# Kernel tuning notes

Hardware: AMD Instinct MI355X
Metric: run time of the kernel (lower is better)

Reference implementation:

```python
import jax, jax.numpy as jnp
import numpy as np

BETA = 0.9       # membrane decay factor
THRESHOLD = 1.0  # firing threshold
ALPHA = 2.0      # atan surrogate slope (snntorch default)

@jax.custom_vjp
def spike(x):
    # Heaviside spike on (mem - threshold)
    return (x > 0).astype(x.dtype)

def _spike_fwd(x):
    return (x > 0).astype(x.dtype), x

def _spike_bwd(x, g):
    # atan surrogate: d spk / d x = (alpha/2) / (1 + (pi/2 * alpha * x)^2)
    return (g * (ALPHA / 2.0) / (1.0 + (jnp.pi / 2.0 * ALPHA * x) ** 2),)

spike.defvjp(_spike_fwd, _spike_bwd)


def snn_forward(x, params):
    """x: (T, B, F_in); params: list of (W[out,in], b[out]).
    Returns (spike_record (T,B,out), final membrane (B,out)).
    Dropout is identity (eval mode). LIF: mem=beta*mem+cur; spk=H(mem-thr); mem-=spk*thr."""
    B = x.shape[1]
    mems0 = tuple(jnp.zeros((B, W.shape[0]), x.dtype) for W, _ in params)

    def step(mems, xt):
        h = xt
        new_mems = []
        for (W, b), m in zip(params, mems):
            cur = h @ W.T + b                 # (B, out)
            m = BETA * m + cur                # leaky integrate
            s = spike(m - THRESHOLD)          # fire
            m = m - s * THRESHOLD             # subtract reset
            new_mems.append(m)
            h = s                             # spikes feed next layer
        return tuple(new_mems), (h, new_mems[-1])

    _, (spks, mem_rec) = jax.lax.scan(step, mems0, x)
    return spks, mem_rec[-1]


def _linear_init(key, out_f, in_f):
    k1, k2 = jax.random.split(key)
    bound = 1.0 / np.sqrt(in_f)
    W = jax.random.uniform(k1, (out_f, in_f), jnp.float32, -bound, bound)
    b = jax.random.uniform(k2, (out_f,), jnp.float32, -bound, bound)
    return W, b


def setup_inputs() -> dict:
    key = jax.random.key(0)
    ks = jax.random.split(key, 4)
    T, B = 25, 256
    sizes = [1024, 2048, 2048, 1024]
    x = jax.random.normal(ks[0], (T, B, sizes[0]), jnp.float32)
    w0, b0 = _linear_init(ks[1], sizes[1], sizes[0])
    w1, b1 = _linear_init(ks[2], sizes[2], sizes[1])
    w2, b2 = _linear_init(ks[3], sizes[3], sizes[2])
    return {"x": x, "w0": w0, "b0": b0, "w1": w1, "b1": b1, "w2": w2, "b2": b2}


def reference(x, w0, b0, w1, b1, w2, b2):
    return snn_forward(x, [(w0, b0), (w1, b1), (w2, b2)])
```

## Files before the change

kernel.cpp:

```cpp
#include <hip/hip_runtime.h>
#include <hip/hip_bf16.h>

typedef __bf16 bf16;
typedef __bf16 bf16x4 __attribute__((ext_vector_type(4)));
typedef __bf16 bf16x8 __attribute__((ext_vector_type(8)));
typedef float  f32x4  __attribute__((ext_vector_type(4)));
typedef signed char i8;
typedef signed char i8x4 __attribute__((ext_vector_type(4)));
typedef int    i32x4 __attribute__((ext_vector_type(4)));

#define DEVFN static __device__ __forceinline__

static constexpr int T_STEPS = 25;
static constexpr int BATCH   = 256;
static constexpr int MROWS   = T_STEPS * BATCH;

DEVFN void llds16(const void* g, void* l) {
    __builtin_amdgcn_global_load_lds(
        (const __attribute__((address_space(1))) void*)g,
        (__attribute__((address_space(3))) void*)l, 16, 0, 0);
}

DEVFN void split3_chunk(const float* src, bf16* p0, bf16* p1, bf16* p2, int i) {
    float4 v = *(const float4*)(src + i);
    float vv[4] = {v.x, v.y, v.z, v.w};
    bf16x4 a, b, c;
#pragma unroll
    for (int k = 0; k < 4; ++k) {
        bf16 h0 = (bf16)vv[k];
        float r1 = vv[k] - (float)h0;
        bf16 h1 = (bf16)r1;
        float r2 = r1 - (float)h1;
        a[k] = h0; b[k] = h1; c[k] = (bf16)r2;
    }
    *(bf16x4*)(p0 + i) = a;
    *(bf16x4*)(p1 + i) = b;
    *(bf16x4*)(p2 + i) = c;
}

DEVFN void spliti8_3(const float* src, i8* p0, i8* p1, i8* p2, int i) {
    float4 v = *(const float4*)(src + i);
    float vv[4] = {v.x, v.y, v.z, v.w};
    i8x4 a, b, c;
#pragma unroll
    for (int k = 0; k < 4; ++k) {
        float t  = vv[k] * 4096.0f;
        float q0 = rintf(t);  float r = t - q0;
        float q1 = rintf(r * 128.0f); r = r * 128.0f - q1;
        float q2 = rintf(r * 128.0f);
        a[k] = (i8)(int)q0; b[k] = (i8)(int)q1; c[k] = (i8)(int)q2;
    }
    *(i8x4*)(p0 + i) = a; *(i8x4*)(p1 + i) = b; *(i8x4*)(p2 + i) = c;
}

DEVFN void spliti8_2(const float* src, i8* p0, i8* p1, int i) {
    float4 v = *(const float4*)(src + i);
    float vv[4] = {v.x, v.y, v.z, v.w};
    i8x4 a, b;
#pragma unroll
    for (int k = 0; k < 4; ++k) {
        float t  = vv[k] * 4096.0f;
        float q0 = rintf(t);  float r = t - q0;
        float q1 = rintf(r * 128.0f);
        a[k] = (i8)(int)q0; b[k] = (i8)(int)q1;
    }
    *(i8x4*)(p0 + i) = a; *(i8x4*)(p1 + i) = b;
}

static constexpr int SB_W0 = 2048;
static constexpr int SB_W1 = 4096;
static constexpr int SB_W2 = 2048;
static constexpr int SB_X  = 6400;

__global__ void split_all(const float* __restrict__ w0, bf16* w0p0, bf16* w0p1, bf16* w0p2,
                          const float* __restrict__ w1, i8* w1q0, i8* w1q1, i8* w1q2,
                          const float* __restrict__ w2, i8* w2q0, i8* w2q1,
                          const float* __restrict__ x,  bf16* xp0,  bf16* xp1,  bf16* xp2) {
    int b = blockIdx.x;
    if (b < SB_W0) {
        split3_chunk(w0, w0p0, w0p1, w0p2, b * 1024 + threadIdx.x * 4);
    } else if (b < SB_W0 + SB_W1) {
        spliti8_3(w1, w1q0, w1q1, w1q2, (b - SB_W0) * 1024 + threadIdx.x * 4);
    } else if (b < SB_W0 + SB_W1 + SB_W2) {
        spliti8_2(w2, w2q0, w2q1, (b - SB_W0 - SB_W1) * 1024 + threadIdx.x * 4);
    } else {
        split3_chunk(x, xp0, xp1, xp2, (b - SB_W0 - SB_W1 - SB_W2) * 1024 + threadIdx.x * 4);
    }
}

DEVFN void mfma16(f32x4 (&acc)[4][4], const bf16x8* a, const bf16x8* b) {
    __builtin_amdgcn_s_setprio(1);
#pragma unroll
    for (int i = 0; i < 4; ++i)
#pragma unroll
        for (int j = 0; j < 4; ++j)
            acc[i][j] = __builtin_amdgcn_mfma_f32_16x16x32_bf16(a[i], b[j], acc[i][j], 0, 0, 0);
    __builtin_amdgcn_s_setprio(0);
}

DEVFN void frag4b(bf16x8* f, const bf16* s, int wrow, int fr, int fkS) {
#pragma unroll
    for (int i = 0; i < 4; ++i)
        f[i] = *(const bf16x8*)((const char*)s + (wrow + i * 16 + fr) * 64 + fkS);
}

__global__ __launch_bounds__(512, 2)
void gemm_l0(const bf16* __restrict__ A0, const bf16* __restrict__ A1,
             const bf16* __restrict__ A2, const bf16* __restrict__ B0,
             const bf16* __restrict__ B1, const bf16* __restrict__ B2,
             const float* __restrict__ bias, float* __restrict__ C,
             int M, int N, int K) {
    constexpr int APL = 256 * 32;
    constexpr int BPL = 128 * 32;
    constexpr int BUF = 3 * APL + 3 * BPL;
    __shared__ __align__(1024) bf16 lds[2 * BUF];

    const int t = threadIdx.x, lane = t & 63, wv = t >> 6;
    const int wm = (wv >> 1) * 64, wn = (wv & 1) * 64;
    const int bm = blockIdx.x * 256, bn = blockIdx.y * 128;
    const int sk = (wv >> 2) & 1;
    const int fr = lane & 15, g = lane >> 4;
    const int fkS = (g ^ ((lane >> 1) & 3)) * 16;
    const int cr = g * 4, cc = fr;

    f32x4 accM[4][4] = {}, accS[4][4] = {};

    auto pA = [&](int p, int i) { return lds + p * BUF + i * APL; };
    auto pB = [&](int p, int i) { return lds + p * BUF + 3 * APL + i * BPL; };

    int offA[2], offB[1];
#pragma unroll
    for (int r = 0; r < 2; ++r) {
        int c = t + r * 512, row = c >> 2, slot = c & 3;
        offA[r] = (bm + row) * K + (slot ^ ((row >> 1) & 3)) * 8;
    }
    {
        int c = t, row = c >> 2, slot = c & 3;
        offB[0] = (bn + row) * K + (slot ^ ((row >> 1) & 3)) * 8;
    }
    auto stA = [&](const bf16* gp, bf16* s, int k0) {
#pragma unroll
        for (int r = 0; r < 2; ++r)
            llds16(gp + offA[r] + k0, (char*)s + ((t + r * 512) >> 6) * 1024);
    };
    auto stB = [&](const bf16* gp, bf16* s, int k0) {
        llds16(gp + offB[0] + k0, (char*)s + (t >> 6) * 1024);
    };

    stA(A0, pA(0, 0), 0); stA(A1, pA(0, 1), 0); stA(A2, pA(0, 2), 0);
    stB(B0, pB(0, 0), 0); stB(B1, pB(0, 1), 0); stB(B2, pB(0, 2), 0);
    __syncthreads();

    const int NT = K / 32;
    int p = 0;
    for (int tt = 0; tt < NT; ++tt, p ^= 1) {
        const int q = p ^ 1, kn = (tt + 1) * 32;
        const bool pf = (tt + 1 < NT);
        bf16x8 a[4], b0f[4], b1f[4], b2f[4];
        if (sk == 0) {
            frag4b(a,   pA(p, 0), wm, fr, fkS);
            frag4b(b0f, pB(p, 0), wn, fr, fkS);
            if (pf) stA(A0, pA(q, 0), kn);
            mfma16(accM, a, b0f);
            if (pf) { stA(A1, pA(q, 1), kn); stA(A2, pA(q, 2), kn); }
            frag4b(b1f, pB(p, 1), wn, fr, fkS);
            mfma16(accS, a, b1f);
            if (pf) { stB(B0, pB(q, 0), kn); stB(B1, pB(q, 1), kn); stB(B2, pB(q, 2), kn); }
            frag4b(b2f, pB(p, 2), wn, fr, fkS);
            mfma16(accS, a, b2f);
            frag4b(a, pA(p, 1), wm, fr, fkS);
            mfma16(accS, a, b0f);
            mfma16(accS, a, b1f);
            frag4b(a, pA(p, 2), wm, fr, fkS);
            mfma16(accS, a, b0f);
        } else {
            frag4b(a,   pA(p, 1), wm, fr, fkS);
            frag4b(b0f, pB(p, 0), wn, fr, fkS);
            if (pf) stA(A0, pA(q, 0), kn);
            mfma16(accS, a, b0f);
            if (pf) { stA(A1, pA(q, 1), kn); stA(A2, pA(q, 2), kn); }
            frag4b(b1f, pB(p, 1), wn, fr, fkS);
            mfma16(accS, a, b1f);
            if (pf) { stB(B0, pB(q, 0), kn); stB(B1, pB(q, 1), kn); stB(B2, pB(q, 2), kn); }
            frag4b(a, pA(p, 2), wm, fr, fkS);
            mfma16(accS, a, b0f);
            frag4b(a, pA(p, 0), wm, fr, fkS);
            mfma16(accM, a, b0f);
            frag4b(b2f, pB(p, 2), wn, fr, fkS);
            mfma16(accS, a, b1f);
            mfma16(accS, a, b2f);
        }
        __syncthreads();
    }

#pragma unroll
    for (int j = 0; j < 4; ++j) {
        int col = bn + wn + j * 16 + cc;
        double bvs = (double)bias[col];
#pragma unroll
        for (int i = 0; i < 4; ++i) {
            int row0 = bm + wm + i * 16 + cr;
#pragma unroll
            for (int r = 0; r < 4; ++r) {
                double v = (double)accM[i][j][r] + (double)accS[i][j][r] + bvs;
                C[(size_t)(row0 + r) * N + col] = (float)v;
            }
        }
    }
}

template <int MODE>
__global__ __launch_bounds__(512, 2)
void gemm_i8(const i8* __restrict__ A, const i8* __restrict__ B0,
             const i8* __restrict__ B1, const i8* __restrict__ B2,
             const float* __restrict__ bias, float* __restrict__ C,
             int M, int N, int K) {
    constexpr int NP  = (MODE == 1) ? 3 : 2;
    constexpr int BN  = (MODE == 1) ? 64 : 128;
    constexpr int WNF = (MODE == 1) ? 2 : 4;
    constexpr int BK  = 128;
    constexpr int APL = 256 * BK;
    constexpr int BPL = BN * BK;
    constexpr int BUF = APL + NP * BPL;
    constexpr int AIT = 4;
    constexpr int BIT = (BN * 8) / 512;
    __shared__ __align__(1024) i8 lds[2 * BUF];

    const int t = threadIdx.x, lane = t & 63, wv = t >> 6;
    const int wm = (wv >> 1) * 64, wn = (wv & 1) * (WNF * 16);
    const int bm = blockIdx.x * 256, bn = blockIdx.y * BN;
    const int fr = lane & 15, g = lane >> 4;
    const int fkA = (g ^ (lane & 7)) * 16;
    const int fkB = ((4 + g) ^ (lane & 7)) * 16;
    const int cr = g * 4, cc = fr;

    i32x4 acc[NP][4][WNF] = {};

    int offA[AIT], offB[BIT];
#pragma unroll
    for (int r = 0; r < AIT; ++r) {
        int c = t + r * 512, row = c >> 3, slot = c & 7;
        offA[r] = (bm + row) * K + (slot ^ (row & 7)) * 16;
    }
#pragma unroll
    for (int r = 0; r < BIT; ++r) {
        int c = t + r * 512, row = c >> 3, slot = c & 7;
        offB[r] = (bn + row) * K + (slot ^ (row & 7)) * 16;
    }
    auto stA = [&](const i8* gp, i8* s, int k0) {
#pragma unroll
        for (int r = 0; r < AIT; ++r)
            llds16(gp + offA[r] + k0, s + ((t + r * 512) >> 6) * 1024);
    };
    auto stB = [&](const i8* gp, i8* s, int k0) {
#pragma unroll
        for (int r = 0; r < BIT; ++r)
            llds16(gp + offB[r] + k0, s + ((t + r * 512) >> 6) * 1024);
    };
    auto pAl = [&](int p) { return lds + p * BUF; };
    auto pBl = [&](int p, int pl) { return lds + p * BUF + APL + pl * BPL; };

    stA(A, pAl(0), 0);
    stB(B0, pBl(0, 0), 0);
    stB(B1, pBl(0, 1), 0);
    if constexpr (NP == 3) stB(B2, pBl(0, 2), 0);
    __syncthreads();

    const int NT = K / BK;
    int p = 0;
    for (int tt = 0; tt < NT; ++tt, p ^= 1) {
        const int q = p ^ 1, kn = (tt + 1) * BK;
        const bool pf = (tt + 1 < NT);
        const i8* sA = pAl(p);
        i32x4 av[4], bvf[NP][WNF];
#pragma unroll
        for (int kh = 0; kh < 2; ++kh) {
            const int fk = kh ? fkB : fkA;
#pragma unroll
            for (int i = 0; i < 4; ++i)
                av[i] = *(const i32x4*)(sA + (wm + i * 16 + fr) * 128 + fk);
            if (kh == 0 && pf) stA(A, pAl(q), kn);
#pragma unroll
            for (int pl = 0; pl < NP; ++pl) {
                const i8* sB = pBl(p, pl);
#pragma unroll
                for (int j = 0; j < WNF; ++j)
                    bvf[pl][j] = *(const i32x4*)(sB + (wn + j * 16 + fr) * 128 + fk);
            }
            if (kh == 0 && pf) {
                stB(B0, pBl(q, 0), kn);
                stB(B1, pBl(q, 1), kn);
                if constexpr (NP == 3) stB(B2, pBl(q, 2), kn);
            }
            __builtin_amdgcn_s_setprio(1);
#pragma unroll
            for (int pl = 0; pl < NP; ++pl)
#pragma unroll
                for (int i = 0; i < 4; ++i)
#pragma unroll
                    for (int j = 0; j < WNF; ++j)
                        acc[pl][i][j] = __builtin_amdgcn_mfma_i32_16x16x64_i8(
                            av[i], bvf[pl][j], acc[pl][i][j], 0, 0, 0);
            __builtin_amdgcn_s_setprio(0);
        }
        __syncthreads();
    }

#pragma unroll
    for (int j = 0; j < WNF; ++j) {
        int col = bn + wn + j * 16 + cc;
        double bvs = (double)bias[col];
#pragma unroll
        for (int i = 0; i < 4; ++i) {
            int row0 = bm + wm + i * 16 + cr;
#pragma unroll
            for (int r = 0; r < 4; ++r) {
                double v = (double)acc[0][i][j][r] + (double)acc[1][i][j][r] * (1.0 / 128.0);
                if constexpr (NP == 3) v += (double)acc[2][i][j][r] * (1.0 / 16384.0);
                C[(size_t)(row0 + r) * N + col] = (float)(v * (1.0 / 4096.0) + bvs);
            }
        }
    }
}

template <int F>
__global__ void lif_hidden(const float* __restrict__ cur, i8* __restrict__ spk) {
    const int tid = blockIdx.x * 256 + threadIdx.x;
    double m = 0.0;
    size_t off = tid;
#pragma unroll
    for (int t = 0; t < T_STEPS; ++t) {
        m = 0.9 * m + (double)cur[off];
        bool s = (m - 1.0) > 0.0;
        spk[off] = s ? (i8)1 : (i8)0;
        if (s) m -= 1.0;
        off += (size_t)BATCH * F;
    }
}

__global__ void lif_out(const float* __restrict__ cur, float* __restrict__ out) {
    const int tid = blockIdx.x * 256 + threadIdx.x;
    double m = 0.0;
    size_t off = tid;
#pragma unroll
    for (int t = 0; t < T_STEPS; ++t) {
        m = 0.9 * m + (double)cur[off];
        bool s = (m - 1.0) > 0.0;
        out[off] = s ? 1.0f : 0.0f;
        if (s) m -= 1.0;
        off += (size_t)BATCH * 1024;
    }
    out[(size_t)T_STEPS * BATCH * 1024 + tid] = (float)m;
}

extern "C" void kernel_launch(void* const* d_in, const int* in_sizes, int n_in,
                              void* d_out, int out_size, void* d_ws, size_t ws_size,
                              hipStream_t stream) {
    const float* xin = (const float*)d_in[0];
    const float* w0  = (const float*)d_in[1];
    const float* b0  = (const float*)d_in[2];
    const float* w1  = (const float*)d_in[3];
    const float* b1  = (const float*)d_in[4];
    const float* w2  = (const float*)d_in[5];
    const float* b2  = (const float*)d_in[6];
    float* out = (float*)d_out;

    constexpr size_t NW0 = 2048 * 1024;
    constexpr size_t NW1 = 2048 * 2048;
    constexpr size_t NW2 = 1024 * 2048;
    constexpr size_t NX  = (size_t)MROWS * 1024;
    constexpr size_t NH  = (size_t)MROWS * 2048;

    char* ws = (char*)d_ws;
    size_t off = 0;
    auto carve = [&](size_t bytes) { char* p = ws + off; off += bytes; return p; };

    i8* w1q0 = (i8*)carve(NW1);
    i8* w1q1 = (i8*)carve(NW1);
    i8* w1q2 = (i8*)carve(NW1);
    i8* w2q0 = (i8*)carve(NW2);
    i8* w2q1 = (i8*)carve(NW2);
    char* pool = carve(2 * NH * 2);
    bf16* w0p0 = (bf16*)pool;
    bf16* w0p1 = w0p0 + NW0;
    bf16* w0p2 = w0p1 + NW0;
    bf16* xp0  = w0p2 + NW0;
    bf16* xp1  = xp0 + NX;
    bf16* xp2  = xp1 + NX;
    i8* s0 = (i8*)pool;
    i8* s1 = s0 + NH;
    float* cur = (float*)carve(NH * 4);
    if (ws_size < off) return;

    split_all<<<SB_W0 + SB_W1 + SB_W2 + SB_X, 256, 0, stream>>>(
        w0, w0p0, w0p1, w0p2, w1, w1q0, w1q1, w1q2,
        w2, w2q0, w2q1, xin, xp0, xp1, xp2);

    gemm_l0<<<dim3(25, 16), 512, 0, stream>>>(xp0, xp1, xp2, w0p0, w0p1, w0p2,
                                              b0, cur, MROWS, 2048, 1024);
    lif_hidden<2048><<<(BATCH * 2048) / 256, 256, 0, stream>>>(cur, s0);

    gemm_i8<1><<<dim3(25, 32), 512, 0, stream>>>(s0, w1q0, w1q1, w1q2,
                                                 b1, cur, MROWS, 2048, 2048);
    lif_hidden<2048><<<(BATCH * 2048) / 256, 256, 0, stream>>>(cur, s1);

    gemm_i8<2><<<dim3(25, 8), 512, 0, stream>>>(s1, w2q0, w2q1, nullptr,
                                                b2, cur, MROWS, 1024, 2048);
    lif_out<<<(BATCH * 1024) / 256, 256, 0, stream>>>(cur, out);
}
```

Before: 412.4 us.

## Replace bf16x3 split layer-0 GEMM with four-plane int8 fixed-point GEMM

Layer 0 now quantizes x and W0 into four int8 planes each (fixed-point scales 16 and 2048, base 128 per plane) instead of three bf16 planes. A new int8 MFMA kernel (16x16x64) computes the ten significant cross-plane products into four int32 accumulators, which are combined in double precision with power-of-two weights. The aim is to use the higher int8 MFMA throughput and halve operand bytes in place of bf16 emulation of fp32. In exchange it adds a fixed-range quantization that assumes bounded input magnitudes (x scaled by 16 must fit in int8), which risks overflow or precision loss for large-valued inputs.

```diff
diff --git a/kernel.cpp b/kernel.cpp
--- a/kernel.cpp
+++ b/kernel.cpp
@@ -2,9 +2,6 @@
 #include <hip/hip_bf16.h>
 
 typedef __bf16 bf16;
-typedef __bf16 bf16x4 __attribute__((ext_vector_type(4)));
-typedef __bf16 bf16x8 __attribute__((ext_vector_type(8)));
-typedef float  f32x4  __attribute__((ext_vector_type(4)));
 typedef signed char i8;
 typedef signed char i8x4 __attribute__((ext_vector_type(4)));
 typedef int    i32x4 __attribute__((ext_vector_type(4)));
@@ -21,21 +18,23 @@
         (__attribute__((address_space(3))) void*)l, 16, 0, 0);
 }
 
-DEVFN void split3_chunk(const float* src, bf16* p0, bf16* p1, bf16* p2, int i) {
+DEVFN void spliti8_4(const float* src, float scale,
+                     i8* p0, i8* p1, i8* p2, i8* p3, int i) {
     float4 v = *(const float4*)(src + i);
     float vv[4] = {v.x, v.y, v.z, v.w};
-    bf16x4 a, b, c;
+    i8x4 a, b, c, d;
 #pragma unroll
     for (int k = 0; k < 4; ++k) {
-        bf16 h0 = (bf16)vv[k];
-        float r1 = vv[k] - (float)h0;
-        bf16 h1 = (bf16)r1;
-        float r2 = r1 - (float)h1;
-        a[k] = h0; b[k] = h1; c[k] = (bf16)r2;
-    }
-    *(bf16x4*)(p0 + i) = a;
-    *(bf16x4*)(p1 + i) = b;
-    *(bf16x4*)(p2 + i) = c;
+        float t  = vv[k] * scale;
+        float q0 = rintf(t);          float r = t - q0;
+        float q1 = rintf(r * 128.0f); r = r * 128.0f - q1;
+        float q2 = rintf(r * 128.0f); r = r * 128.0f - q2;
+        float q3 = rintf(r * 128.0f);
+        a[k] = (i8)(int)q0; b[k] = (i8)(int)q1;
+        c[k] = (i8)(int)q2; d[k] = (i8)(int)q3;
+    }
+    *(i8x4*)(p0 + i) = a; *(i8x4*)(p1 + i) = b;
+    *(i8x4*)(p2 + i) = c; *(i8x4*)(p3 + i) = d;
 }
 
 DEVFN void spliti8_3(const float* src, i8* p0, i8* p1, i8* p2, int i) {
@@ -72,138 +71,163 @@
 static constexpr int SB_W2 = 2048;
 static constexpr int SB_X  = 6400;
 
-__global__ void split_all(const float* __restrict__ w0, bf16* w0p0, bf16* w0p1, bf16* w0p2,
+__global__ void split_all(const float* __restrict__ w0, i8* w0q0, i8* w0q1, i8* w0q2, i8* w0q3,
                           const float* __restrict__ w1, i8* w1q0, i8* w1q1, i8* w1q2,
                           const float* __restrict__ w2, i8* w2q0, i8* w2q1,
-                          const float* __restrict__ x,  bf16* xp0,  bf16* xp1,  bf16* xp2) {
+                          const float* __restrict__ x,  i8* xq0, i8* xq1, i8* xq2, i8* xq3) {
     int b = blockIdx.x;
     if (b < SB_W0) {
-        split3_chunk(w0, w0p0, w0p1, w0p2, b * 1024 + threadIdx.x * 4);
+        spliti8_4(w0, 2048.0f, w0q0, w0q1, w0q2, w0q3, b * 1024 + threadIdx.x * 4);
     } else if (b < SB_W0 + SB_W1) {
         spliti8_3(w1, w1q0, w1q1, w1q2, (b - SB_W0) * 1024 + threadIdx.x * 4);
     } else if (b < SB_W0 + SB_W1 + SB_W2) {
         spliti8_2(w2, w2q0, w2q1, (b - SB_W0 - SB_W1) * 1024 + threadIdx.x * 4);
     } else {
-        split3_chunk(x, xp0, xp1, xp2, (b - SB_W0 - SB_W1 - SB_W2) * 1024 + threadIdx.x * 4);
-    }
-}
-
-DEVFN void mfma16(f32x4 (&acc)[4][4], const bf16x8* a, const bf16x8* b) {
-    __builtin_amdgcn_s_setprio(1);
-#pragma unroll
-    for (int i = 0; i < 4; ++i)
-#pragma unroll
-        for (int j = 0; j < 4; ++j)
-            acc[i][j] = __builtin_amdgcn_mfma_f32_16x16x32_bf16(a[i], b[j], acc[i][j], 0, 0, 0);
-    __builtin_amdgcn_s_setprio(0);
-}
-
-DEVFN void frag4b(bf16x8* f, const bf16* s, int wrow, int fr, int fkS) {
-#pragma unroll
-    for (int i = 0; i < 4; ++i)
-        f[i] = *(const bf16x8*)((const char*)s + (wrow + i * 16 + fr) * 64 + fkS);
+        spliti8_4(x, 16.0f, xq0, xq1, xq2, xq3,
+                  (b - SB_W0 - SB_W1 - SB_W2) * 1024 + threadIdx.x * 4);
+    }
 }
 
 __global__ __launch_bounds__(512, 2)
-void gemm_l0(const bf16* __restrict__ A0, const bf16* __restrict__ A1,
-             const bf16* __restrict__ A2, const bf16* __restrict__ B0,
-             const bf16* __restrict__ B1, const bf16* __restrict__ B2,
-             const float* __restrict__ bias, float* __restrict__ C,
-             int M, int N, int K) {
-    constexpr int APL = 256 * 32;
-    constexpr int BPL = 128 * 32;
-    constexpr int BUF = 3 * APL + 3 * BPL;
-    __shared__ __align__(1024) bf16 lds[2 * BUF];
+void gemm_l0i8(const i8* __restrict__ X0, const i8* __restrict__ X1,
+               const i8* __restrict__ X2, const i8* __restrict__ X3,
+               const i8* __restrict__ W0, const i8* __restrict__ W1,
+               const i8* __restrict__ W2, const i8* __restrict__ W3,
+               const float* __restrict__ bias, float* __restrict__ C,
+               int M, int N, int K) {
+    constexpr int APL = 256 * 64;
+    constexpr int BPL = 64 * 64;
+    constexpr int BUF = 4 * APL + 4 * BPL;
+    __shared__ __align__(1024) i8 lds[2 * BUF];
 
     const int t = threadIdx.x, lane = t & 63, wv = t >> 6;
-    const int wm = (wv >> 1) * 64, wn = (wv & 1) * 64;
-    const int bm = blockIdx.x * 256, bn = blockIdx.y * 128;
+    const int wm = (wv >> 1) * 64, wn = (wv & 1) * 32;
+    const int bm = blockIdx.x * 256, bn = blockIdx.y * 64;
     const int sk = (wv >> 2) & 1;
     const int fr = lane & 15, g = lane >> 4;
-    const int fkS = (g ^ ((lane >> 1) & 3)) * 16;
+    const int fk = (g ^ ((lane >> 1) & 3)) * 16;
     const int cr = g * 4, cc = fr;
 
-    f32x4 accM[4][4] = {}, accS[4][4] = {};
+    i32x4 acc0[4][2] = {}, acc1[4][2] = {}, acc2[4][2] = {}, acc3[4][2] = {};
 
     auto pA = [&](int p, int i) { return lds + p * BUF + i * APL; };
-    auto pB = [&](int p, int i) { return lds + p * BUF + 3 * APL + i * BPL; };
-
-    int offA[2], offB[1];
+    auto pB = [&](int p, int i) { return lds + p * BUF + 4 * APL + i * BPL; };
+
+    int offA[2], offB;
 #pragma unroll
     for (int r = 0; r < 2; ++r) {
         int c = t + r * 512, row = c >> 2, slot = c & 3;
-        offA[r] = (bm + row) * K + (slot ^ ((row >> 1) & 3)) * 8;
-    }
-    {
-        int c = t, row = c >> 2, slot = c & 3;
-        offB[0] = (bn + row) * K + (slot ^ ((row >> 1) & 3)) * 8;
-    }
-    auto stA = [&](const bf16* gp, bf16* s, int k0) {
+        offA[r] = (bm + row) * K + (slot ^ ((row >> 1) & 3)) * 16;
+    }
+    { int c = t & 255, row = c >> 2, slot = c & 3;
+      offB = (bn + row) * K + (slot ^ ((row >> 1) & 3)) * 16; }
+
+    auto stA = [&](const i8* gp, i8* s, int k0) {
 #pragma unroll
         for (int r = 0; r < 2; ++r)
-            llds16(gp + offA[r] + k0, (char*)s + ((t + r * 512) >> 6) * 1024);
+            llds16(gp + offA[r] + k0, s + ((t + r * 512) >> 6) * 1024);
     };
-    auto stB = [&](const bf16* gp, bf16* s, int k0) {
-        llds16(gp + offB[0] + k0, (char*)s + (t >> 6) * 1024);
+    auto stB2 = [&](const i8* gl, const i8* gh, i8* sl, i8* sh, int k0) {
+        const i8* gp = (t < 256) ? gl : gh;
+        i8* s = (t < 256) ? sl : sh;
+        llds16(gp + offB + k0, s + ((t & 255) >> 6) * 1024);
     };
 
-    stA(A0, pA(0, 0), 0); stA(A1, pA(0, 1), 0); stA(A2, pA(0, 2), 0);
-    stB(B0, pB(0, 0), 0); stB(B1, pB(0, 1), 0); stB(B2, pB(0, 2), 0);
+    stA(X0, pA(0, 0), 0); stA(X1, pA(0, 1), 0);
+    stA(X2, pA(0, 2), 0); stA(X3, pA(0, 3), 0);
+    stB2(W0, W1, pB(0, 0), pB(0, 1), 0);
+    stB2(W2, W3, pB(0, 2), pB(0, 3), 0);
     __syncthreads();
 
-    const int NT = K / 32;
+    const int NT = K / 64;
     int p = 0;
     for (int tt = 0; tt < NT; ++tt, p ^= 1) {
-        const int q = p ^ 1, kn = (tt + 1) * 32;
+        const int q = p ^ 1, kn = (tt + 1) * 64;
         const bool pf = (tt + 1 < NT);
-        bf16x8 a[4], b0f[4], b1f[4], b2f[4];
+
+        i32x4 av[4], bv0[2], bv1[2], bv2[2], bv3[2];
+        auto ldA = [&](int pl) {
+            const i8* s = pA(p, pl);
+#pragma unroll
+            for (int ri = 0; ri < 4; ++ri)
+                av[ri] = *(const i32x4*)(s + (wm + ri * 16 + fr) * 64 + fk);
+        };
+        auto ldB = [&](int pl, i32x4 (&f)[2]) {
+            const i8* s = pB(p, pl);
+#pragma unroll
+            for (int j = 0; j < 2; ++j)
+                f[j] = *(const i32x4*)(s + (wn + j * 16 + fr) * 64 + fk);
+        };
+        auto pass = [&](const i32x4 (&bj)[2], i32x4 (&ac)[4][2]) {
+            __builtin_amdgcn_s_setprio(1);
+#pragma unroll
+            for (int ri = 0; ri < 4; ++ri)
+#pragma unroll
+                for (int j = 0; j < 2; ++j)
+                    ac[ri][j] = __builtin_amdgcn_mfma_i32_16x16x64_i8(
+                        av[ri], bj[j], ac[ri][j], 0, 0, 0);
+            __builtin_amdgcn_s_setprio(0);
+        };
+
+        ldB(0, bv0); ldB(1, bv1); ldB(2, bv2); ldB(3, bv3);
         if (sk == 0) {
-            frag4b(a,   pA(p, 0), wm, fr, fkS);
-            frag4b(b0f, pB(p, 0), wn, fr, fkS);
-            if (pf) stA(A0, pA(q, 0), kn);
-            mfma16(accM, a, b0f);
-            if (pf) { stA(A1, pA(q, 1), kn); stA(A2, pA(q, 2), kn); }
-            frag4b(b1f, pB(p, 1), wn, fr, fkS);
-            mfma16(accS, a, b1f);
-            if (pf) { stB(B0, pB(q, 0), kn); stB(B1, pB(q, 1), kn); stB(B2, pB(q, 2), kn); }
-            frag4b(b2f, pB(p, 2), wn, fr, fkS);
-            mfma16(accS, a, b2f);
-            frag4b(a, pA(p, 1), wm, fr, fkS);
-            mfma16(accS, a, b0f);
-            mfma16(accS, a, b1f);
-            frag4b(a, pA(p, 2), wm, fr, fkS);
-            mfma16(accS, a, b0f);
+            ldA(0);
+            if (pf) stA(X0, pA(q, 0), kn);
+            pass(bv0, acc0);
+            if (pf) { stA(X1, pA(q, 1), kn); stA(X2, pA(q, 2), kn); }
+            pass(bv1, acc1);
+            if (pf) stA(X3, pA(q, 3), kn);
+            pass(bv2, acc2);
+            if (pf) stB2(W0, W1, pB(q, 0), pB(q, 1), kn);
+            pass(bv3, acc3);
+            ldA(1);
+            if (pf) stB2(W2, W3, pB(q, 2), pB(q, 3), kn);
+            pass(bv0, acc1);
+            pass(bv1, acc2);
+            pass(bv2, acc3);
+            ldA(2);
+            pass(bv0, acc2);
+            pass(bv1, acc3);
+            ldA(3);
+            pass(bv0, acc3);
         } else {
-            frag4b(a,   pA(p, 1), wm, fr, fkS);
-            frag4b(b0f, pB(p, 0), wn, fr, fkS);
-            if (pf) stA(A0, pA(q, 0), kn);
-            mfma16(accS, a, b0f);
-            if (pf) { stA(A1, pA(q, 1), kn); stA(A2, pA(q, 2), kn); }
-            frag4b(b1f, pB(p, 1), wn, fr, fkS);
-            mfma16(accS, a, b1f);
-            if (pf) { stB(B0, pB(q, 0), kn); stB(B1, pB(q, 1), kn); stB(B2, pB(q, 2), kn); }
-            frag4b(a, pA(p, 2), wm, fr, fkS);
-            mfma16(accS, a, b0f);
-            frag4b(a, pA(p, 0), wm, fr, fkS);
-            mfma16(accM, a, b0f);
-            frag4b(b2f, pB(p, 2), wn, fr, fkS);
-            mfma16(accS, a, b1f);
-            mfma16(accS, a, b2f);
+            ldA(2);
+            if (pf) stA(X0, pA(q, 0), kn);
+            pass(bv0, acc2);
+            if (pf) { stA(X1, pA(q, 1), kn); stA(X2, pA(q, 2), kn); }
+            pass(bv1, acc3);
+            ldA(3);
+            if (pf) stA(X3, pA(q, 3), kn);
+            pass(bv0, acc3);
+            ldA(0);
+            if (pf) stB2(W0, W1, pB(q, 0), pB(q, 1), kn);
+            pass(bv0, acc0);
+            if (pf) stB2(W2, W3, pB(q, 2), pB(q, 3), kn);
+            pass(bv1, acc1);
+            pass(bv2, acc2);
+            pass(bv3, acc3);
+            ldA(1);
+            pass(bv0, acc1);
+            pass(bv1, acc2);
+            pass(bv2, acc3);
         }
         __syncthreads();
     }
 
 #pragma unroll
-    for (int j = 0; j < 4; ++j) {
+    for (int j = 0; j < 2; ++j) {
         int col = bn + wn + j * 16 + cc;
         double bvs = (double)bias[col];
 #pragma unroll
-        for (int i = 0; i < 4; ++i) {
-            int row0 = bm + wm + i * 16 + cr;
+        for (int ri = 0; ri < 4; ++ri) {
+            int row0 = bm + wm + ri * 16 + cr;
 #pragma unroll
             for (int r = 0; r < 4; ++r) {
-                double v = (double)accM[i][j][r] + (double)accS[i][j][r] + bvs;
-                C[(size_t)(row0 + r) * N + col] = (float)v;
+                double v = (double)acc0[ri][j][r]
+                         + (double)acc1[ri][j][r] * (1.0 / 128.0)
+                         + (double)acc2[ri][j][r] * (1.0 / 16384.0)
+                         + (double)acc3[ri][j][r] * (1.0 / 2097152.0);
+                C[(size_t)(row0 + r) * N + col] = (float)(v * (1.0 / 32768.0) + bvs);
             }
         }
     }
@@ -381,23 +405,26 @@
     i8* w2q0 = (i8*)carve(NW2);
     i8* w2q1 = (i8*)carve(NW2);
     char* pool = carve(2 * NH * 2);
-    bf16* w0p0 = (bf16*)pool;
-    bf16* w0p1 = w0p0 + NW0;
-    bf16* w0p2 = w0p1 + NW0;
-    bf16* xp0  = w0p2 + NW0;
-    bf16* xp1  = xp0 + NX;
-    bf16* xp2  = xp1 + NX;
+    i8* xq0  = (i8*)pool;
+    i8* xq1  = xq0 + NX;
+    i8* xq2  = xq1 + NX;
+    i8* xq3  = xq2 + NX;
+    i8* w0q0 = xq3 + NX;
+    i8* w0q1 = w0q0 + NW0;
+    i8* w0q2 = w0q1 + NW0;
+    i8* w0q3 = w0q2 + NW0;
     i8* s0 = (i8*)pool;
     i8* s1 = s0 + NH;
     float* cur = (float*)carve(NH * 4);
     if (ws_size < off) return;
 
     split_all<<<SB_W0 + SB_W1 + SB_W2 + SB_X, 256, 0, stream>>>(
-        w0, w0p0, w0p1, w0p2, w1, w1q0, w1q1, w1q2,
-        w2, w2q0, w2q1, xin, xp0, xp1, xp2);
-
-    gemm_l0<<<dim3(25, 16), 512, 0, stream>>>(xp0, xp1, xp2, w0p0, w0p1, w0p2,
-                                              b0, cur, MROWS, 2048, 1024);
+        w0, w0q0, w0q1, w0q2, w0q3, w1, w1q0, w1q1, w1q2,
+        w2, w2q0, w2q1, xin, xq0, xq1, xq2, xq3);
+
+    gemm_l0i8<<<dim3(25, 32), 512, 0, stream>>>(xq0, xq1, xq2, xq3,
+                                                w0q0, w0q1, w0q2, w0q3,
+                                                b0, cur, MROWS, 2048, 1024);
     lif_hidden<2048><<<(BATCH * 2048) / 256, 256, 0, stream>>>(cur, s0);
 
     gemm_i8<1><<<dim3(25, 32), 512, 0, stream>>>(s0, w1q0, w1q1, w1q2,
```

Measured after the change: 431.2 us. 1.05x slower.
